# Kernel tuning notes

Measured on AMD Instinct MI355X. Metric: run time of the kernel, lower is better.

The kernel has to match this reference:

```python
import jax, jax.numpy as jnp
import numpy as np

D_MODEL = 1024
N_HEADS = 16
D_K = D_MODEL // N_HEADS
B, T = 4, 2048


def setup_inputs() -> dict:
    key = jax.random.key(0)
    ks = jax.random.split(key, 12)
    s = 1.0 / np.sqrt(D_MODEL)
    inp = {
        "query": jax.random.normal(ks[0], (B, T, D_MODEL), dtype=jnp.float32),
        "key": jax.random.normal(ks[1], (B, T, D_MODEL), dtype=jnp.float32),
        "value": jax.random.normal(ks[2], (B, T, D_MODEL), dtype=jnp.float32),
        # causal mask, broadcastable over batch and heads
        "mask": jnp.tril(jnp.ones((T, T), dtype=bool))[None, None, :, :],
        "W_q": jax.random.uniform(ks[3], (D_MODEL, D_MODEL), jnp.float32, -s, s),
        "b_q": jnp.zeros((D_MODEL,), jnp.float32),
        "W_k": jax.random.uniform(ks[4], (D_MODEL, D_MODEL), jnp.float32, -s, s),
        "b_k": jnp.zeros((D_MODEL,), jnp.float32),
        "W_v": jax.random.uniform(ks[5], (D_MODEL, D_MODEL), jnp.float32, -s, s),
        "b_v": jnp.zeros((D_MODEL,), jnp.float32),
        "W_o": jax.random.uniform(ks[6], (D_MODEL, D_MODEL), jnp.float32, -s, s),
        "b_o": jnp.zeros((D_MODEL,), jnp.float32),
    }
    return inp


def _split_heads(x):
    b, t, _ = x.shape
    return x.reshape(b, t, N_HEADS, D_K).transpose(0, 2, 1, 3)  # [B,H,T,Dk]


def reference(query, key, value, mask, W_q, b_q, W_k, b_k, W_v, b_v, W_o, b_o):
    q = _split_heads(query @ W_q.T + b_q)
    k = _split_heads(key @ W_k.T + b_k)
    v = _split_heads(value @ W_v.T + b_v)
    scale = 1.0 / jnp.sqrt(jnp.asarray(D_K, q.dtype))
    scores = jnp.einsum("bhqd,bhkd->bhqk", q, k) * scale  # [B,H,Tq,Tk]
    scores = jnp.where(mask, scores, jnp.asarray(-jnp.inf, scores.dtype))
    attn = jax.nn.softmax(scores, axis=-1)
    out = jnp.einsum("bhqk,bhkd->bhqd", attn, v)
    out = out.transpose(0, 2, 1, 3).reshape(query.shape[0], query.shape[1], D_MODEL)
    return out @ W_o.T + b_o
```

## Files before the change

### kernel.cpp

```cpp
#include <hip/hip_runtime.h>
#include <stdint.h>
#include <stddef.h>


typedef __attribute__((ext_vector_type(4))) float f32x4;
typedef __attribute__((ext_vector_type(8))) _Float16 f16x8;
typedef __attribute__((ext_vector_type(4))) _Float16 f16x4;

#define DEV __device__ __forceinline__

constexpr int BATCH = 4, SEQ = 2048, NH = 16, DK = 64, DM = 1024;
constexpr int MROWS = BATCH * SEQ;
constexpr float QSCALE = 0.125f * 1.4426950408889634f;

DEV void async16(const void* g, void* l) {
  __builtin_amdgcn_global_load_lds(
      (const __attribute__((address_space(1))) unsigned int*)g,
      (__attribute__((address_space(3))) unsigned int*)l, 16, 0, 0);
}

__global__ void cvt_w_kernel(const float* __restrict__ w0, const float* __restrict__ w1,
                             const float* __restrict__ w2, const float* __restrict__ w3,
                             _Float16* __restrict__ o0, _Float16* __restrict__ o1,
                             _Float16* __restrict__ o2, _Float16* __restrict__ o3) {
  size_t i = (size_t)blockIdx.x * blockDim.x + threadIdx.x;
  const float* ws[4] = {w0, w1, w2, w3};
  _Float16* os[4] = {o0, o1, o2, o3};
#pragma unroll
  for (int m = 0; m < 4; m++) {
    f32x4 x = *(const f32x4*)(ws[m] + i * 4);
    f16x4 h;
#pragma unroll
    for (int j = 0; j < 4; j++) h[j] = (_Float16)x[j];
    *(f16x4*)(os[m] + i * 4) = h;
  }
}

__global__ void cvt_act_kernel(const float* __restrict__ a0, const float* __restrict__ a1,
                               const float* __restrict__ a2, _Float16* __restrict__ o0,
                               _Float16* __restrict__ o1, _Float16* __restrict__ o2) {
  size_t i = (size_t)blockIdx.x * blockDim.x + threadIdx.x;
  const float* as[3] = {a0, a1, a2};
  _Float16* os[3] = {o0, o1, o2};
#pragma unroll
  for (int m = 0; m < 3; m++) {
    f32x4 x = *(const f32x4*)(as[m] + i * 4);
    f16x4 h;
#pragma unroll
    for (int j = 0; j < 4; j++) h[j] = (_Float16)x[j];
    *(f16x4*)(os[m] + i * 4) = h;
  }
}

struct QKVPtrs {
  const float* a32[3];
  const _Float16* a16[3];
  const _Float16* w[3];
  const float* bias[3];
  _Float16* out[3];
};

DEV void stage_g16(const _Float16* __restrict__ src, int k0, _Float16* dst, int tid) {
  const int wave = tid >> 6;
#pragma unroll
  for (int it = 0; it < 4; it++) {
    int idx = it * 256 + tid;
    int row = idx >> 3, seg = idx & 7;
    async16(src + (size_t)row * DM + k0 + ((seg ^ (row & 7)) << 3),
            (char*)dst + (size_t)(it * 256 + wave * 64) * 16);
  }
}

DEV void stage_f32(const float* __restrict__ src, int k0, _Float16* dst, int tid) {
#pragma unroll
  for (int it = 0; it < 4; it++) {
    int idx = it * 256 + tid;
    int row = idx >> 3, seg = idx & 7;
    const float* g = src + (size_t)row * DM + k0 + seg * 8;
    f32x4 x0 = *(const f32x4*)g;
    f32x4 x1 = *(const f32x4*)(g + 4);
    f16x8 h;
#pragma unroll
    for (int j = 0; j < 4; j++) { h[j] = (_Float16)x0[j]; h[4 + j] = (_Float16)x1[j]; }
    *(f16x8*)&dst[row * 64 + ((seg ^ (row & 7)) << 3)] = h;
  }
}

template <bool AH>
__global__ __launch_bounds__(256) void gemm_qkv_kernel(QKVPtrs P) {
  constexpr int K = DM;
  __shared__ __align__(16) _Float16 smem[4 * 128 * 64];
  const int z = blockIdx.z;
  const _Float16* Bw = P.w[z];
  const int tid = threadIdx.x;
  const int wave = tid >> 6, lane = tid & 63;
  const int quad = lane >> 4, l16 = lane & 15;
  const int wm = wave >> 1, wn = wave & 1;
  const int m0 = blockIdx.x * 128, n0 = blockIdx.y * 128;
  const float scale = (z == 0) ? QSCALE : 1.0f;

  const _Float16* Bg = Bw + (size_t)n0 * K;
  const _Float16* Ag16 = AH ? P.a16[z] + (size_t)m0 * K : nullptr;
  const float* Ag32 = AH ? nullptr : P.a32[z] + (size_t)m0 * K;

  const f32x4 zero4 = {0.f, 0.f, 0.f, 0.f};
  f32x4 acc[4][4];
#pragma unroll
  for (int mt = 0; mt < 4; mt++)
#pragma unroll
    for (int nt = 0; nt < 4; nt++) acc[mt][nt] = zero4;

  float bv[4];
#pragma unroll
  for (int nt = 0; nt < 4; nt++) bv[nt] = P.bias[z][n0 + wn * 64 + nt * 16 + l16];

  stage_g16(Bg, 0, smem + 8192, tid);
  if (AH) stage_g16(Ag16, 0, smem, tid);
  else    stage_f32(Ag32, 0, smem, tid);
  __syncthreads();

  for (int kt = 0; kt < K / 64; kt++) {
    const int boff = (kt & 1) ? 16384 : 0;
    const _Float16* Asc = smem + boff;
    const _Float16* Bsc = smem + 8192 + boff;
    if (kt + 1 < K / 64) {
      const int k0 = (kt + 1) * 64;
      const int poff = boff ^ 16384;
      stage_g16(Bg, k0, smem + 8192 + poff, tid);
      if (AH) stage_g16(Ag16, k0, smem + poff, tid);
      else    stage_f32(Ag32, k0, smem + poff, tid);
    }
    __builtin_amdgcn_s_setprio(1);
#pragma unroll
    for (int ks = 0; ks < 2; ks++) {
      f16x8 af[4], bfr[4];
#pragma unroll
      for (int mt = 0; mt < 4; mt++) {
        int r = wm * 64 + mt * 16 + l16;
        af[mt] = *(const f16x8*)&Asc[r * 64 + (((ks * 4 + quad) ^ (r & 7)) << 3)];
      }
#pragma unroll
      for (int nt = 0; nt < 4; nt++) {
        int r = wn * 64 + nt * 16 + l16;
        bfr[nt] = *(const f16x8*)&Bsc[r * 64 + (((ks * 4 + quad) ^ (r & 7)) << 3)];
      }
#pragma unroll
      for (int mt = 0; mt < 4; mt++)
#pragma unroll
        for (int nt = 0; nt < 4; nt++)
          acc[mt][nt] = __builtin_amdgcn_mfma_f32_16x16x32_f16(af[mt], bfr[nt], acc[mt][nt], 0, 0, 0);
    }
    __builtin_amdgcn_s_setprio(0);
    __syncthreads();
  }

  _Float16* Ct = smem;
  const int b = m0 >> 11, tbase = m0 & (SEQ - 1);
  if (z < 2) {
#pragma unroll
    for (int mt = 0; mt < 4; mt++)
#pragma unroll
      for (int nt = 0; nt < 4; nt++)
#pragma unroll
        for (int i = 0; i < 4; i++)
          Ct[(wm * 64 + mt * 16 + quad * 4 + i) * 144 + wn * 64 + nt * 16 + l16] =
              (_Float16)((acc[mt][nt][i] + bv[nt]) * scale);
  } else {
#pragma unroll
    for (int mt = 0; mt < 4; mt++)
#pragma unroll
      for (int nt = 0; nt < 4; nt++)
#pragma unroll
        for (int i = 0; i < 4; i++)
          Ct[(wn * 64 + nt * 16 + l16) * 144 + wm * 64 + mt * 16 + quad * 4 + i] =
              (_Float16)(acc[mt][nt][i] + bv[nt]);
  }
  __syncthreads();
  _Float16* out = P.out[z];
  if (z < 2) {
    const int row = tid >> 1, coff = (tid & 1) * 32;
#pragma unroll
    for (int hh = 0; hh < 2; hh++) {
      int h = (n0 >> 6) + hh;
      size_t gb = ((size_t)(b * NH + h) * SEQ + tbase) * 64 + (size_t)tid * 32;
#pragma unroll
      for (int k2 = 0; k2 < 4; k2++)
        *(f16x8*)&out[gb + k2 * 8] =
            *(const f16x8*)&Ct[row * 144 + hh * 64 + coff + k2 * 8];
    }
  } else {
#pragma unroll
    for (int k2 = 0; k2 < 8; k2++) {
      int c = k2 * 256 + tid;
      int n = c >> 4, s2 = c & 15;
      int h = (n0 + n) >> 6, d = (n0 + n) & (DK - 1);
      size_t gb = ((size_t)(b * NH + h) * DK + d) * SEQ + tbase + s2 * 8;
      *(f16x8*)&out[gb] = *(const f16x8*)&Ct[n * 144 + s2 * 8];
    }
  }
}

__global__ __launch_bounds__(256) void gemm_out_kernel(
    const _Float16* __restrict__ Ah, const _Float16* __restrict__ Bw,
    const float* __restrict__ bias, float* __restrict__ Cp) {
  constexpr int K = DM;
  __shared__ __align__(16) _Float16 smem[4 * 128 * 64];
  const int tid = threadIdx.x;
  const int wave = tid >> 6, lane = tid & 63;
  const int quad = lane >> 4, l16 = lane & 15;
  const int wm = wave >> 1, wn = wave & 1;
  const int m0 = blockIdx.x * 128, n0 = blockIdx.y * 128;

  const _Float16* Bg = Bw + (size_t)n0 * K;
  const _Float16* Ag = Ah + (size_t)m0 * K;

  const f32x4 zero4 = {0.f, 0.f, 0.f, 0.f};
  f32x4 acc[4][4];
#pragma unroll
  for (int mt = 0; mt < 4; mt++)
#pragma unroll
    for (int nt = 0; nt < 4; nt++) acc[mt][nt] = zero4;

  float bv[4];
#pragma unroll
  for (int nt = 0; nt < 4; nt++) bv[nt] = bias[n0 + wn * 64 + nt * 16 + l16];

  stage_g16(Bg, 0, smem + 8192, tid);
  stage_g16(Ag, 0, smem, tid);
  __syncthreads();

  for (int kt = 0; kt < K / 64; kt++) {
    const int boff = (kt & 1) ? 16384 : 0;
    const _Float16* Asc = smem + boff;
    const _Float16* Bsc = smem + 8192 + boff;
    if (kt + 1 < K / 64) {
      const int k0 = (kt + 1) * 64;
      const int poff = boff ^ 16384;
      stage_g16(Bg, k0, smem + 8192 + poff, tid);
      stage_g16(Ag, k0, smem + poff, tid);
    }
    __builtin_amdgcn_s_setprio(1);
#pragma unroll
    for (int ks = 0; ks < 2; ks++) {
      f16x8 af[4], bfr[4];
#pragma unroll
      for (int mt = 0; mt < 4; mt++) {
        int r = wm * 64 + mt * 16 + l16;
        af[mt] = *(const f16x8*)&Asc[r * 64 + (((ks * 4 + quad) ^ (r & 7)) << 3)];
      }
#pragma unroll
      for (int nt = 0; nt < 4; nt++) {
        int r = wn * 64 + nt * 16 + l16;
        bfr[nt] = *(const f16x8*)&Bsc[r * 64 + (((ks * 4 + quad) ^ (r & 7)) << 3)];
      }
#pragma unroll
      for (int mt = 0; mt < 4; mt++)
#pragma unroll
        for (int nt = 0; nt < 4; nt++)
          acc[mt][nt] = __builtin_amdgcn_mfma_f32_16x16x32_f16(af[mt], bfr[nt], acc[mt][nt], 0, 0, 0);
    }
    __builtin_amdgcn_s_setprio(0);
    __syncthreads();
  }
#pragma unroll
  for (int mt = 0; mt < 4; mt++)
#pragma unroll
    for (int nt = 0; nt < 4; nt++)
#pragma unroll
      for (int i = 0; i < 4; i++) {
        int m = m0 + wm * 64 + mt * 16 + quad * 4 + i;
        int n = n0 + wn * 64 + nt * 16 + l16;
        Cp[(size_t)m * DM + n] = acc[mt][nt][i] + bv[nt];
      }
}

__global__ __launch_bounds__(256, 2) void attn_kernel(
    const _Float16* __restrict__ Q, const _Float16* __restrict__ Kt,
    const _Float16* __restrict__ V, _Float16* __restrict__ O) {
  __shared__ __align__(16) _Float16 Ks[2 * 128 * 64];
  __shared__ __align__(16) _Float16 Vs[2 * 64 * 128];
  const int tid = threadIdx.x;
  const int wave = tid >> 6, lane = tid & 63, quad = lane >> 4, l16 = lane & 15;
  const int bh = blockIdx.y;
  const size_t base = (size_t)bh * SEQ * DK;
  const int b = bh >> 4, h = bh & 15;
  const f32x4 zero4 = {0.f, 0.f, 0.f, 0.f};

  int koffs[2], voffs[8];
#pragma unroll
  for (int ks = 0; ks < 2; ks++) koffs[ks] = ((ks * 4 + quad) ^ (l16 & 7)) << 3;
#pragma unroll
  for (int jj = 0; jj < 8; jj++)
    voffs[jj] = (((jj * 2 + (quad >> 1)) ^ l16) << 3) + (quad & 1) * 4;

  for (int p = 0; p < 2; p++) {
    const int qt = (p == 0) ? (int)blockIdx.x : 15 - (int)blockIdx.x;
    const int t0 = qt * 128;

    f16x8 qf[2][2];
#pragma unroll
    for (int mt = 0; mt < 2; mt++)
#pragma unroll
      for (int ks = 0; ks < 2; ks++)
        qf[mt][ks] = *(const f16x8*)(Q + base + (size_t)(t0 + wave * 32 + mt * 16 + l16) * DK +
                                     ks * 32 + quad * 8);

    f32x4 oacc[2][4];
#pragma unroll
    for (int mt = 0; mt < 2; mt++)
#pragma unroll
      for (int nt = 0; nt < 4; nt++) oacc[mt][nt] = zero4;
    float mrow[2] = {-1e30f, -1e30f}, lrow[2] = {0.f, 0.f};

    {
      const int wbase = wave * 64;
#pragma unroll
      for (int it = 0; it < 4; it++) {
        int idx = it * 256 + tid;
        int row = idx >> 3, seg = idx & 7;
        async16(Kt + base + (size_t)row * 64 + ((seg ^ (row & 7)) << 3),
                (char*)Ks + (size_t)(it * 256 + wbase) * 16);
      }
#pragma unroll
      for (int it = 0; it < 4; it++) {
        int idx = it * 256 + tid;
        int d = idx >> 4, g = idx & 15;
        async16(V + base + ((size_t)d << 11) + ((g ^ (d & 15)) << 3),
                (char*)Vs + (size_t)(it * 256 + wbase) * 16);
      }
    }
    __syncthreads();

    for (int j = 0; j <= qt; j++) {
      const int koff = (j & 1) ? 8192 : 0;
      const _Float16* Kb = Ks + koff;
      const _Float16* Vb = Vs + koff;
      if (j < qt) {
        const int poff = koff ^ 8192;
        const int wbase = wave * 64;
        const int jn = (j + 1) * 128;
#pragma unroll
        for (int it = 0; it < 4; it++) {
          int idx = it * 256 + tid;
          int row = idx >> 3, seg = idx & 7;
          async16(Kt + base + (size_t)(jn + row) * 64 + ((seg ^ (row & 7)) << 3),
                  (char*)(Ks + poff) + (size_t)(it * 256 + wbase) * 16);
        }
#pragma unroll
        for (int it = 0; it < 4; it++) {
          int idx = it * 256 + tid;
          int d = idx >> 4, g = idx & 15;
          async16(V + base + ((size_t)d << 11) + jn + ((g ^ (d & 15)) << 3),
                  (char*)(Vs + poff) + (size_t)(it * 256 + wbase) * 16);
        }
      }

      f32x4 s[2][8];
      __builtin_amdgcn_s_setprio(1);
#pragma unroll
      for (int nt = 0; nt < 8; nt++) {
        int rb = (nt * 16 + l16) * 64;
        f16x8 kf0 = *(const f16x8*)&Kb[rb + koffs[0]];
        f16x8 kf1 = *(const f16x8*)&Kb[rb + koffs[1]];
#pragma unroll
        for (int mt = 0; mt < 2; mt++) {
          f32x4 zz = zero4;
          zz = __builtin_amdgcn_mfma_f32_16x16x32_f16(kf0, qf[mt][0], zz, 0, 0, 0);
          zz = __builtin_amdgcn_mfma_f32_16x16x32_f16(kf1, qf[mt][1], zz, 0, 0, 0);
          s[mt][nt] = zz;
        }
      }
      __builtin_amdgcn_s_setprio(0);
      if (j == qt) {
#pragma unroll
        for (int mt = 0; mt < 2; mt++) {
          int qloc = wave * 32 + mt * 16 + l16;
#pragma unroll
          for (int nt = 0; nt < 8; nt++)
#pragma unroll
            for (int i = 0; i < 4; i++)
              if (nt * 16 + quad * 4 + i > qloc) s[mt][nt][i] = -1e30f;
        }
      }
#pragma unroll
      for (int mt = 0; mt < 2; mt++) {
        float mx = mrow[mt];
#pragma unroll
        for (int nt = 0; nt < 8; nt++)
#pragma unroll
          for (int i = 0; i < 4; i++) mx = fmaxf(mx, s[mt][nt][i]);
        mx = fmaxf(mx, __shfl_xor(mx, 16));
        mx = fmaxf(mx, __shfl_xor(mx, 32));
        float alpha = __builtin_exp2f(mrow[mt] - mx);
        mrow[mt] = mx;
        float rs = 0.f;
#pragma unroll
        for (int nt = 0; nt < 8; nt++)
#pragma unroll
          for (int i = 0; i < 4; i++) {
            float pv = __builtin_exp2f(s[mt][nt][i] - mx);
            s[mt][nt][i] = pv;
            rs += pv;
          }
        rs += __shfl_xor(rs, 16);
        rs += __shfl_xor(rs, 32);
        lrow[mt] = lrow[mt] * alpha + rs;
#pragma unroll
        for (int i = 0; i < 4; i++) {
          float ab = __shfl(alpha, quad * 4 + i);
#pragma unroll
          for (int nt = 0; nt < 4; nt++) oacc[mt][nt][i] *= ab;
        }
      }
      __builtin_amdgcn_s_setprio(1);
#pragma unroll
      for (int jj = 0; jj < 8; jj++) {
        f16x4 pf[2];
#pragma unroll
        for (int mt = 0; mt < 2; mt++) {
          f16x4 t;
#pragma unroll
          for (int i = 0; i < 4; i++) t[i] = (_Float16)s[mt][jj][i];
          pf[mt] = t;
        }
#pragma unroll
        for (int nt = 0; nt < 4; nt++) {
          f16x4 vb = *(const f16x4*)&Vb[(nt * 16 + l16) * 128 + voffs[jj]];
#pragma unroll
          for (int mt = 0; mt < 2; mt++)
            oacc[mt][nt] = __builtin_amdgcn_mfma_f32_16x16x16f16(pf[mt], vb, oacc[mt][nt], 0, 0, 0);
        }
      }
      __builtin_amdgcn_s_setprio(0);
      __syncthreads();
    }
#pragma unroll
    for (int mt = 0; mt < 2; mt++) {
      float linv = 1.0f / lrow[mt];
#pragma unroll
      for (int i = 0; i < 4; i++) {
        float lb = __shfl(linv, quad * 4 + i);
        int t = t0 + wave * 32 + mt * 16 + quad * 4 + i;
#pragma unroll
        for (int nt = 0; nt < 4; nt++) {
          int d = nt * 16 + l16;
          O[((size_t)(b * SEQ + t) << 10) + h * 64 + d] = (_Float16)(oacc[mt][nt][i] * lb);
        }
      }
    }
  }
}

extern "C" void kernel_launch(void* const* d_in, const int* in_sizes, int n_in,
                              void* d_out, int out_size, void* d_ws, size_t ws_size,
                              hipStream_t stream) {
  const float* query = (const float*)d_in[0];
  const float* key_  = (const float*)d_in[1];
  const float* value = (const float*)d_in[2];
  const float* W_q = (const float*)d_in[4];
  const float* b_q = (const float*)d_in[5];
  const float* W_k = (const float*)d_in[6];
  const float* b_k = (const float*)d_in[7];
  const float* W_v = (const float*)d_in[8];
  const float* b_v = (const float*)d_in[9];
  const float* W_o = (const float*)d_in[10];
  const float* b_o = (const float*)d_in[11];

  constexpr size_t WEL = (size_t)DM * DM;
  constexpr size_t MEL = (size_t)MROWS * DM;
  _Float16* ws = (_Float16*)d_ws;
  _Float16* wq = ws;
  _Float16* wk = wq + WEL;
  _Float16* wv = wk + WEL;
  _Float16* wo = wv + WEL;

  const bool big = ws_size >= (size_t)(4 * WEL + 6 * MEL) * sizeof(_Float16);

  QKVPtrs P;
  P.a32[0] = query; P.a32[1] = key_; P.a32[2] = value;
  P.w[0] = wq; P.w[1] = wk; P.w[2] = wv;
  P.bias[0] = b_q; P.bias[1] = b_k; P.bias[2] = b_v;

  cvt_w_kernel<<<dim3((unsigned)(WEL / 4 / 256)), 256, 0, stream>>>(
      W_q, W_k, W_v, W_o, wq, wk, wv, wo);

  _Float16 *qb, *kb, *vb, *ab;
  if (big) {
    _Float16* qh = wo + WEL;
    _Float16* kh = qh + MEL;
    _Float16* vh = kh + MEL;
    qb = vh + MEL; kb = qb + MEL; vb = kb + MEL;
    ab = qh;
    P.a16[0] = qh; P.a16[1] = kh; P.a16[2] = vh;
    P.out[0] = qb; P.out[1] = kb; P.out[2] = vb;
    cvt_act_kernel<<<dim3((unsigned)(MEL / 4 / 256)), 256, 0, stream>>>(
        query, key_, value, qh, kh, vh);
    gemm_qkv_kernel<true><<<dim3(MROWS / 128, DM / 128, 3), 256, 0, stream>>>(P);
  } else {
    qb = wo + WEL; kb = qb + MEL; vb = kb + MEL; ab = vb + MEL;
    P.a16[0] = P.a16[1] = P.a16[2] = nullptr;
    P.out[0] = qb; P.out[1] = kb; P.out[2] = vb;
    gemm_qkv_kernel<false><<<dim3(MROWS / 128, DM / 128, 3), 256, 0, stream>>>(P);
  }

  attn_kernel<<<dim3(8, BATCH * NH), 256, 0, stream>>>(qb, kb, vb, ab);

  gemm_out_kernel<<<dim3(MROWS / 128, DM / 128), 256, 0, stream>>>(ab, wo, b_o, (float*)d_out);
}
```

Measured before the change: 335.4 us.

## Restructure attention: one query tile per block, register-staged V, lazy rescale

The attention kernel now launches one block per query tile (16 per head) instead of pairing two tiles per block, with a rotated tile order so heavy and light blocks interleave. V is loaded into registers and written to a single LDS buffer between barriers instead of async double-buffering, which cuts shared memory so the launch bound can rise to 3 blocks per CU. The softmax skips rescaling the accumulator unless the running max grows by more than 8 (log2 units), and probabilities are packed with cvt_pkrtz. The trade-offs are an extra barrier per iteration, exposed V load latency, and round-toward-zero fp16 conversion of probabilities.

```diff
diff --git a/kernel.cpp b/kernel.cpp
--- a/kernel.cpp
+++ b/kernel.cpp
@@ -6,6 +6,8 @@
 typedef __attribute__((ext_vector_type(4))) float f32x4;
 typedef __attribute__((ext_vector_type(8))) _Float16 f16x8;
 typedef __attribute__((ext_vector_type(4))) _Float16 f16x4;
+typedef __attribute__((ext_vector_type(2))) __fp16 hf2;
+typedef __attribute__((ext_vector_type(4))) __fp16 hf4;
 
 #define DEV __device__ __forceinline__
 
@@ -274,16 +276,19 @@
       }
 }
 
-__global__ __launch_bounds__(256, 2) void attn_kernel(
+__global__ __launch_bounds__(256, 3) void attn_kernel(
     const _Float16* __restrict__ Q, const _Float16* __restrict__ Kt,
     const _Float16* __restrict__ V, _Float16* __restrict__ O) {
   __shared__ __align__(16) _Float16 Ks[2 * 128 * 64];
-  __shared__ __align__(16) _Float16 Vs[2 * 64 * 128];
+  __shared__ __align__(16) _Float16 Vs[64 * 128];
   const int tid = threadIdx.x;
   const int wave = tid >> 6, lane = tid & 63, quad = lane >> 4, l16 = lane & 15;
   const int bh = blockIdx.y;
   const size_t base = (size_t)bh * SEQ * DK;
   const int b = bh >> 4, h = bh & 15;
+  const int qt = 15 - (((int)blockIdx.x + ((int)blockIdx.y >> 2)) & 15);
+  const int t0 = qt * 128;
+  const int nT = qt + 1;
   const f32x4 zero4 = {0.f, 0.f, 0.f, 0.f};
 
   int koffs[2], voffs[8];
@@ -293,118 +298,104 @@
   for (int jj = 0; jj < 8; jj++)
     voffs[jj] = (((jj * 2 + (quad >> 1)) ^ l16) << 3) + (quad & 1) * 4;
 
-  for (int p = 0; p < 2; p++) {
-    const int qt = (p == 0) ? (int)blockIdx.x : 15 - (int)blockIdx.x;
-    const int t0 = qt * 128;
-
-    f16x8 qf[2][2];
-#pragma unroll
-    for (int mt = 0; mt < 2; mt++)
-#pragma unroll
-      for (int ks = 0; ks < 2; ks++)
-        qf[mt][ks] = *(const f16x8*)(Q + base + (size_t)(t0 + wave * 32 + mt * 16 + l16) * DK +
-                                     ks * 32 + quad * 8);
-
-    f32x4 oacc[2][4];
-#pragma unroll
-    for (int mt = 0; mt < 2; mt++)
-#pragma unroll
-      for (int nt = 0; nt < 4; nt++) oacc[mt][nt] = zero4;
-    float mrow[2] = {-1e30f, -1e30f}, lrow[2] = {0.f, 0.f};
-
-    {
-      const int wbase = wave * 64;
-#pragma unroll
-      for (int it = 0; it < 4; it++) {
-        int idx = it * 256 + tid;
-        int row = idx >> 3, seg = idx & 7;
-        async16(Kt + base + (size_t)row * 64 + ((seg ^ (row & 7)) << 3),
-                (char*)Ks + (size_t)(it * 256 + wbase) * 16);
-      }
-#pragma unroll
-      for (int it = 0; it < 4; it++) {
-        int idx = it * 256 + tid;
-        int d = idx >> 4, g = idx & 15;
-        async16(V + base + ((size_t)d << 11) + ((g ^ (d & 15)) << 3),
-                (char*)Vs + (size_t)(it * 256 + wbase) * 16);
-      }
-    }
-    __syncthreads();
-
-    for (int j = 0; j <= qt; j++) {
-      const int koff = (j & 1) ? 8192 : 0;
-      const _Float16* Kb = Ks + koff;
-      const _Float16* Vb = Vs + koff;
-      if (j < qt) {
-        const int poff = koff ^ 8192;
-        const int wbase = wave * 64;
-        const int jn = (j + 1) * 128;
-#pragma unroll
-        for (int it = 0; it < 4; it++) {
-          int idx = it * 256 + tid;
-          int row = idx >> 3, seg = idx & 7;
-          async16(Kt + base + (size_t)(jn + row) * 64 + ((seg ^ (row & 7)) << 3),
-                  (char*)(Ks + poff) + (size_t)(it * 256 + wbase) * 16);
-        }
-#pragma unroll
-        for (int it = 0; it < 4; it++) {
-          int idx = it * 256 + tid;
-          int d = idx >> 4, g = idx & 15;
-          async16(V + base + ((size_t)d << 11) + jn + ((g ^ (d & 15)) << 3),
-                  (char*)(Vs + poff) + (size_t)(it * 256 + wbase) * 16);
-        }
-      }
-
-      f32x4 s[2][8];
-      __builtin_amdgcn_s_setprio(1);
-#pragma unroll
-      for (int nt = 0; nt < 8; nt++) {
-        int rb = (nt * 16 + l16) * 64;
-        f16x8 kf0 = *(const f16x8*)&Kb[rb + koffs[0]];
-        f16x8 kf1 = *(const f16x8*)&Kb[rb + koffs[1]];
-#pragma unroll
-        for (int mt = 0; mt < 2; mt++) {
-          f32x4 zz = zero4;
-          zz = __builtin_amdgcn_mfma_f32_16x16x32_f16(kf0, qf[mt][0], zz, 0, 0, 0);
-          zz = __builtin_amdgcn_mfma_f32_16x16x32_f16(kf1, qf[mt][1], zz, 0, 0, 0);
-          s[mt][nt] = zz;
-        }
-      }
-      __builtin_amdgcn_s_setprio(0);
-      if (j == qt) {
-#pragma unroll
-        for (int mt = 0; mt < 2; mt++) {
-          int qloc = wave * 32 + mt * 16 + l16;
-#pragma unroll
-          for (int nt = 0; nt < 8; nt++)
-#pragma unroll
-            for (int i = 0; i < 4; i++)
-              if (nt * 16 + quad * 4 + i > qloc) s[mt][nt][i] = -1e30f;
-        }
-      }
+  f16x8 qf[2][2];
+#pragma unroll
+  for (int mt = 0; mt < 2; mt++)
+#pragma unroll
+    for (int ks = 0; ks < 2; ks++)
+      qf[mt][ks] = *(const f16x8*)(Q + base + (size_t)(t0 + wave * 32 + mt * 16 + l16) * DK +
+                                   ks * 32 + quad * 8);
+
+  f32x4 oacc[2][4];
+#pragma unroll
+  for (int mt = 0; mt < 2; mt++)
+#pragma unroll
+    for (int nt = 0; nt < 4; nt++) oacc[mt][nt] = zero4;
+  float mrow[2] = {-1e30f, -1e30f}, lrow[2] = {0.f, 0.f};
+
+  f16x8 vr[4];
+
+  auto stageK = [&](int j, int off) {
+#pragma unroll
+    for (int it = 0; it < 4; it++) {
+      int idx = it * 256 + tid;
+      int row = idx >> 3, seg = idx & 7;
+      async16(Kt + base + (size_t)(j * 128 + row) * 64 + ((seg ^ (row & 7)) << 3),
+              (char*)(Ks + off) + (size_t)(it * 256 + wave * 64) * 16);
+    }
+  };
+  auto loadV = [&](int j) {
+#pragma unroll
+    for (int it = 0; it < 4; it++) {
+      int idx = it * 256 + tid;
+      int d = idx >> 4, g = idx & 15;
+      vr[it] = *(const f16x8*)(V + base + ((size_t)d << 11) + (size_t)j * 128 +
+                               ((g ^ (d & 15)) << 3));
+    }
+  };
+  auto writeV = [&]() {
+#pragma unroll
+    for (int it = 0; it < 4; it++) {
+      int idx = it * 256 + tid;
+      int d = idx >> 4, g = idx & 15;
+      *(f16x8*)&Vs[d * 128 + g * 8] = vr[it];
+    }
+  };
+
+  stageK(0, 0);
+  loadV(0);
+  writeV();
+  __syncthreads();
+
+  for (int j = 0; j < nT; j++) {
+    const int koff = (j & 1) * 8192;
+    const _Float16* Kb = Ks + koff;
+    if (j + 1 < nT) {
+      stageK(j + 1, koff ^ 8192);
+      loadV(j + 1);
+    }
+
+    f32x4 s[2][8];
+    __builtin_amdgcn_s_setprio(1);
+#pragma unroll
+    for (int nt = 0; nt < 8; nt++) {
+      int rb = (nt * 16 + l16) * 64;
+      f16x8 kf0 = *(const f16x8*)&Kb[rb + koffs[0]];
+      f16x8 kf1 = *(const f16x8*)&Kb[rb + koffs[1]];
 #pragma unroll
       for (int mt = 0; mt < 2; mt++) {
-        float mx = mrow[mt];
+        f32x4 zz = zero4;
+        zz = __builtin_amdgcn_mfma_f32_16x16x32_f16(kf0, qf[mt][0], zz, 0, 0, 0);
+        zz = __builtin_amdgcn_mfma_f32_16x16x32_f16(kf1, qf[mt][1], zz, 0, 0, 0);
+        s[mt][nt] = zz;
+      }
+    }
+    __builtin_amdgcn_s_setprio(0);
+    if (j == qt) {
+#pragma unroll
+      for (int mt = 0; mt < 2; mt++) {
+        int qloc = wave * 32 + mt * 16 + l16;
 #pragma unroll
         for (int nt = 0; nt < 8; nt++)
 #pragma unroll
-          for (int i = 0; i < 4; i++) mx = fmaxf(mx, s[mt][nt][i]);
-        mx = fmaxf(mx, __shfl_xor(mx, 16));
-        mx = fmaxf(mx, __shfl_xor(mx, 32));
+          for (int i = 0; i < 4; i++)
+            if (nt * 16 + quad * 4 + i > qloc) s[mt][nt][i] = -1e30f;
+      }
+    }
+#pragma unroll
+    for (int mt = 0; mt < 2; mt++) {
+      float tmax = s[mt][0][0];
+#pragma unroll
+      for (int nt = 0; nt < 8; nt++)
+#pragma unroll
+        for (int i = 0; i < 4; i++) tmax = fmaxf(tmax, s[mt][nt][i]);
+      tmax = fmaxf(tmax, __shfl_xor(tmax, 16));
+      tmax = fmaxf(tmax, __shfl_xor(tmax, 32));
+      if (__any(tmax > mrow[mt] + 8.0f)) {
+        float mx = fmaxf(mrow[mt], tmax);
         float alpha = __builtin_exp2f(mrow[mt] - mx);
         mrow[mt] = mx;
-        float rs = 0.f;
-#pragma unroll
-        for (int nt = 0; nt < 8; nt++)
-#pragma unroll
-          for (int i = 0; i < 4; i++) {
-            float pv = __builtin_exp2f(s[mt][nt][i] - mx);
-            s[mt][nt][i] = pv;
-            rs += pv;
-          }
-        rs += __shfl_xor(rs, 16);
-        rs += __shfl_xor(rs, 32);
-        lrow[mt] = lrow[mt] * alpha + rs;
+        lrow[mt] *= alpha;
 #pragma unroll
         for (int i = 0; i < 4; i++) {
           float ab = __shfl(alpha, quad * 4 + i);
@@ -412,40 +403,57 @@
           for (int nt = 0; nt < 4; nt++) oacc[mt][nt][i] *= ab;
         }
       }
-      __builtin_amdgcn_s_setprio(1);
-#pragma unroll
-      for (int jj = 0; jj < 8; jj++) {
-        f16x4 pf[2];
-#pragma unroll
-        for (int mt = 0; mt < 2; mt++) {
-          f16x4 t;
-#pragma unroll
-          for (int i = 0; i < 4; i++) t[i] = (_Float16)s[mt][jj][i];
-          pf[mt] = t;
+      float mx = mrow[mt];
+      float rs = 0.f;
+#pragma unroll
+      for (int nt = 0; nt < 8; nt++)
+#pragma unroll
+        for (int i = 0; i < 4; i++) {
+          float pv = __builtin_exp2f(s[mt][nt][i] - mx);
+          s[mt][nt][i] = pv;
+          rs += pv;
         }
-#pragma unroll
-        for (int nt = 0; nt < 4; nt++) {
-          f16x4 vb = *(const f16x4*)&Vb[(nt * 16 + l16) * 128 + voffs[jj]];
-#pragma unroll
-          for (int mt = 0; mt < 2; mt++)
-            oacc[mt][nt] = __builtin_amdgcn_mfma_f32_16x16x16f16(pf[mt], vb, oacc[mt][nt], 0, 0, 0);
-        }
-      }
-      __builtin_amdgcn_s_setprio(0);
+      rs += __shfl_xor(rs, 16);
+      rs += __shfl_xor(rs, 32);
+      lrow[mt] += rs;
+    }
+    __builtin_amdgcn_s_setprio(1);
+#pragma unroll
+    for (int jj = 0; jj < 8; jj++) {
+      f16x4 pf[2];
+#pragma unroll
+      for (int mt = 0; mt < 2; mt++) {
+        hf2 lo = __builtin_amdgcn_cvt_pkrtz(s[mt][jj][0], s[mt][jj][1]);
+        hf2 hi = __builtin_amdgcn_cvt_pkrtz(s[mt][jj][2], s[mt][jj][3]);
+        hf4 cat = __builtin_shufflevector(lo, hi, 0, 1, 2, 3);
+        pf[mt] = __builtin_bit_cast(f16x4, cat);
+      }
+#pragma unroll
+      for (int nt = 0; nt < 4; nt++) {
+        f16x4 vb = *(const f16x4*)&Vs[(nt * 16 + l16) * 128 + voffs[jj]];
+#pragma unroll
+        for (int mt = 0; mt < 2; mt++)
+          oacc[mt][nt] = __builtin_amdgcn_mfma_f32_16x16x16f16(pf[mt], vb, oacc[mt][nt], 0, 0, 0);
+      }
+    }
+    __builtin_amdgcn_s_setprio(0);
+    if (j + 1 < nT) {
       __syncthreads();
-    }
-#pragma unroll
-    for (int mt = 0; mt < 2; mt++) {
-      float linv = 1.0f / lrow[mt];
-#pragma unroll
-      for (int i = 0; i < 4; i++) {
-        float lb = __shfl(linv, quad * 4 + i);
-        int t = t0 + wave * 32 + mt * 16 + quad * 4 + i;
-#pragma unroll
-        for (int nt = 0; nt < 4; nt++) {
-          int d = nt * 16 + l16;
-          O[((size_t)(b * SEQ + t) << 10) + h * 64 + d] = (_Float16)(oacc[mt][nt][i] * lb);
-        }
+      writeV();
+      __syncthreads();
+    }
+  }
+#pragma unroll
+  for (int mt = 0; mt < 2; mt++) {
+    float linv = 1.0f / lrow[mt];
+#pragma unroll
+    for (int i = 0; i < 4; i++) {
+      float lb = __shfl(linv, quad * 4 + i);
+      int t = t0 + wave * 32 + mt * 16 + quad * 4 + i;
+#pragma unroll
+      for (int nt = 0; nt < 4; nt++) {
+        int d = nt * 16 + l16;
+        O[((size_t)(b * SEQ + t) << 10) + h * 64 + d] = (_Float16)(oacc[mt][nt][i] * lb);
       }
     }
   }
@@ -503,7 +511,7 @@
     gemm_qkv_kernel<false><<<dim3(MROWS / 128, DM / 128, 3), 256, 0, stream>>>(P);
   }
 
-  attn_kernel<<<dim3(8, BATCH * NH), 256, 0, stream>>>(qb, kb, vb, ab);
+  attn_kernel<<<dim3(16, BATCH * NH), 256, 0, stream>>>(qb, kb, vb, ab);
 
   gemm_out_kernel<<<dim3(MROWS / 128, DM / 128), 256, 0, stream>>>(ab, wo, b_o, (float*)d_out);
 }
```

After: 408.7 us. 21.8% more time.

## Process paired causal query tiles concurrently with two wave groups sharing K/V staging

Applied to the files above, without the earlier changes.

The attention kernel now launches 512 threads per block: two groups of four waves each handle a different query tile (a late tile 8+r and an early tile 7-r) at the same time, rather than looping over the pair one after the other. Both groups share a single double-buffered K/V LDS stream, so each K/V tile is loaded once for both query tiles, and the early group simply idles on iterations past its diagonal. The pairing is also rotated by head index to spread work. This trades the sequential per-block loop for more waves per block and shared loads, at the cost of idle waves in the early group and higher register pressure under launch bounds of 512 threads with 4 blocks.

```diff
diff --git a/kernel.cpp b/kernel.cpp
--- a/kernel.cpp
+++ b/kernel.cpp
@@ -274,16 +274,22 @@
       }
 }
 
-__global__ __launch_bounds__(256, 2) void attn_kernel(
+__global__ __launch_bounds__(512, 4) void attn_kernel(
     const _Float16* __restrict__ Q, const _Float16* __restrict__ Kt,
     const _Float16* __restrict__ V, _Float16* __restrict__ O) {
   __shared__ __align__(16) _Float16 Ks[2 * 128 * 64];
   __shared__ __align__(16) _Float16 Vs[2 * 64 * 128];
   const int tid = threadIdx.x;
   const int wave = tid >> 6, lane = tid & 63, quad = lane >> 4, l16 = lane & 15;
+  const int grp = wave >> 2, w4 = wave & 3;
   const int bh = blockIdx.y;
   const size_t base = (size_t)bh * SEQ * DK;
   const int b = bh >> 4, h = bh & 15;
+  const int r = ((int)blockIdx.x + bh) & 7;
+  const int qtA = 8 + r;
+  const int qt = grp ? (7 - r) : qtA;
+  const int t0 = qt * 128;
+  const int nT = qtA + 1;
   const f32x4 zero4 = {0.f, 0.f, 0.f, 0.f};
 
   int koffs[2], voffs[8];
@@ -293,68 +299,54 @@
   for (int jj = 0; jj < 8; jj++)
     voffs[jj] = (((jj * 2 + (quad >> 1)) ^ l16) << 3) + (quad & 1) * 4;
 
-  for (int p = 0; p < 2; p++) {
-    const int qt = (p == 0) ? (int)blockIdx.x : 15 - (int)blockIdx.x;
-    const int t0 = qt * 128;
-
-    f16x8 qf[2][2];
-#pragma unroll
-    for (int mt = 0; mt < 2; mt++)
-#pragma unroll
-      for (int ks = 0; ks < 2; ks++)
-        qf[mt][ks] = *(const f16x8*)(Q + base + (size_t)(t0 + wave * 32 + mt * 16 + l16) * DK +
-                                     ks * 32 + quad * 8);
-
-    f32x4 oacc[2][4];
-#pragma unroll
-    for (int mt = 0; mt < 2; mt++)
-#pragma unroll
-      for (int nt = 0; nt < 4; nt++) oacc[mt][nt] = zero4;
-    float mrow[2] = {-1e30f, -1e30f}, lrow[2] = {0.f, 0.f};
-
-    {
-      const int wbase = wave * 64;
-#pragma unroll
-      for (int it = 0; it < 4; it++) {
-        int idx = it * 256 + tid;
-        int row = idx >> 3, seg = idx & 7;
-        async16(Kt + base + (size_t)row * 64 + ((seg ^ (row & 7)) << 3),
-                (char*)Ks + (size_t)(it * 256 + wbase) * 16);
-      }
-#pragma unroll
-      for (int it = 0; it < 4; it++) {
-        int idx = it * 256 + tid;
-        int d = idx >> 4, g = idx & 15;
-        async16(V + base + ((size_t)d << 11) + ((g ^ (d & 15)) << 3),
-                (char*)Vs + (size_t)(it * 256 + wbase) * 16);
-      }
-    }
-    __syncthreads();
-
-    for (int j = 0; j <= qt; j++) {
-      const int koff = (j & 1) ? 8192 : 0;
-      const _Float16* Kb = Ks + koff;
-      const _Float16* Vb = Vs + koff;
-      if (j < qt) {
-        const int poff = koff ^ 8192;
-        const int wbase = wave * 64;
-        const int jn = (j + 1) * 128;
-#pragma unroll
-        for (int it = 0; it < 4; it++) {
-          int idx = it * 256 + tid;
-          int row = idx >> 3, seg = idx & 7;
-          async16(Kt + base + (size_t)(jn + row) * 64 + ((seg ^ (row & 7)) << 3),
-                  (char*)(Ks + poff) + (size_t)(it * 256 + wbase) * 16);
-        }
-#pragma unroll
-        for (int it = 0; it < 4; it++) {
-          int idx = it * 256 + tid;
-          int d = idx >> 4, g = idx & 15;
-          async16(V + base + ((size_t)d << 11) + jn + ((g ^ (d & 15)) << 3),
-                  (char*)(Vs + poff) + (size_t)(it * 256 + wbase) * 16);
-        }
-      }
-
+  f16x8 qf[2][2];
+#pragma unroll
+  for (int mt = 0; mt < 2; mt++)
+#pragma unroll
+    for (int ks = 0; ks < 2; ks++)
+      qf[mt][ks] = *(const f16x8*)(Q + base + (size_t)(t0 + w4 * 32 + mt * 16 + l16) * DK +
+                                   ks * 32 + quad * 8);
+
+  f32x4 oacc[2][4];
+#pragma unroll
+  for (int mt = 0; mt < 2; mt++)
+#pragma unroll
+    for (int nt = 0; nt < 4; nt++) oacc[mt][nt] = zero4;
+  float mrow[2] = {-1e30f, -1e30f}, lrow[2] = {0.f, 0.f};
+
+  auto stageK = [&](int j, int off) {
+#pragma unroll
+    for (int it = 0; it < 2; it++) {
+      int idx = it * 512 + tid;
+      int row = idx >> 3, seg = idx & 7;
+      async16(Kt + base + (size_t)(j * 128 + row) * 64 + ((seg ^ (row & 7)) << 3),
+              (char*)(Ks + off) + (size_t)(it * 512 + wave * 64) * 16);
+    }
+  };
+  auto stageV = [&](int j, int off) {
+#pragma unroll
+    for (int it = 0; it < 2; it++) {
+      int idx = it * 512 + tid;
+      int d = idx >> 4, g = idx & 15;
+      async16(V + base + ((size_t)d << 11) + (size_t)j * 128 + ((g ^ (d & 15)) << 3),
+              (char*)(Vs + off) + (size_t)(it * 512 + wave * 64) * 16);
+    }
+  };
+
+  stageK(0, 0);
+  stageV(0, 0);
+  __syncthreads();
+
+  for (int j = 0; j < nT; j++) {
+    const int koff = (j & 1) * 8192;
+    const _Float16* Kb = Ks + koff;
+    const _Float16* Vb = Vs + koff;
+    if (j + 1 < nT) {
+      stageK(j + 1, koff ^ 8192);
+      stageV(j + 1, koff ^ 8192);
+    }
+
+    if (j <= qt) {
       f32x4 s[2][8];
       __builtin_amdgcn_s_setprio(1);
 #pragma unroll
@@ -374,7 +366,7 @@
       if (j == qt) {
 #pragma unroll
         for (int mt = 0; mt < 2; mt++) {
-          int qloc = wave * 32 + mt * 16 + l16;
+          int qloc = w4 * 32 + mt * 16 + l16;
 #pragma unroll
           for (int nt = 0; nt < 8; nt++)
 #pragma unroll
@@ -432,20 +424,20 @@
         }
       }
       __builtin_amdgcn_s_setprio(0);
-      __syncthreads();
-    }
-#pragma unroll
-    for (int mt = 0; mt < 2; mt++) {
-      float linv = 1.0f / lrow[mt];
-#pragma unroll
-      for (int i = 0; i < 4; i++) {
-        float lb = __shfl(linv, quad * 4 + i);
-        int t = t0 + wave * 32 + mt * 16 + quad * 4 + i;
-#pragma unroll
-        for (int nt = 0; nt < 4; nt++) {
-          int d = nt * 16 + l16;
-          O[((size_t)(b * SEQ + t) << 10) + h * 64 + d] = (_Float16)(oacc[mt][nt][i] * lb);
-        }
+    }
+    __syncthreads();
+  }
+#pragma unroll
+  for (int mt = 0; mt < 2; mt++) {
+    float linv = 1.0f / lrow[mt];
+#pragma unroll
+    for (int i = 0; i < 4; i++) {
+      float lb = __shfl(linv, quad * 4 + i);
+      int t = t0 + w4 * 32 + mt * 16 + quad * 4 + i;
+#pragma unroll
+      for (int nt = 0; nt < 4; nt++) {
+        int d = nt * 16 + l16;
+        O[((size_t)(b * SEQ + t) << 10) + h * 64 + d] = (_Float16)(oacc[mt][nt][i] * lb);
       }
     }
   }
@@ -503,7 +495,7 @@
     gemm_qkv_kernel<false><<<dim3(MROWS / 128, DM / 128, 3), 256, 0, stream>>>(P);
   }
 
-  attn_kernel<<<dim3(8, BATCH * NH), 256, 0, stream>>>(qb, kb, vb, ab);
+  attn_kernel<<<dim3(8, BATCH * NH), 512, 0, stream>>>(qb, kb, vb, ab);
 
   gemm_out_kernel<<<dim3(MROWS / 128, DM / 128), 256, 0, stream>>>(ab, wo, b_o, (float*)d_out);
 }
```

Result: slower. 459.7 us (+37.1%).
